# Performance work log

Hardware: AMD Instinct MI355X
Metric: run time of the kernel (lower is better)

The kernel has to match this reference:

```python
import jax, jax.numpy as jnp
import numpy as np

NEURONS = 4096
K = 512

def setup_inputs() -> dict:
    key = jax.random.key(0)
    s = jax.random.normal(key, (16384, NEURONS), dtype=jnp.float32)
    return {"s": s}

def reference(s) -> jnp.ndarray:
    # Original: sort each row ascending, zero the smallest (neurons - k) entries,
    # i.e. keep only the k largest values per row. With continuous random inputs
    # (no ties) this equals thresholding at the k-th largest value per row.
    topk_vals, _ = jax.lax.top_k(s, K)          # [B, K], descending
    thresh = topk_vals[:, -1:]                   # k-th largest per row, [B, 1]
    return jnp.where(s >= thresh, s, jnp.zeros((), dtype=s.dtype))
```

## Files before the change

### kernel.cpp

```cpp
#include <hip/hip_runtime.h>

#define ROWS 16384
#define COLS 4096
#define KSEL 512
#define THREADS 256
#define NCOPY0 8
#define HSTRIDE 260

__device__ __forceinline__ unsigned map_f(float f) {
    unsigned u = __float_as_uint(f);
    return u ^ (0x80000000u | (unsigned)((int)u >> 31));
}
__device__ __forceinline__ float unmap_f(unsigned m) {
    return __uint_as_float(m ^ (0x80000000u | ~(unsigned)((int)m >> 31)));
}

__device__ __forceinline__ void select_digit(unsigned n0, unsigned n1, unsigned n2,
                                             unsigned n3, int lane, int shift,
                                             unsigned& prefix, unsigned& kk) {
    unsigned ls3 = n3, ls2 = n3 + n2, ls1 = ls2 + n1, tot = ls1 + n0;
    unsigned S = tot;
#pragma unroll
    for (int off = 1; off < 64; off <<= 1) {
        unsigned o = __shfl(S, lane + off);
        S += (lane + off < 64) ? o : 0u;
    }
    const unsigned R = S - tot;
    const unsigned S3 = R + ls3, S2 = R + ls2, S1 = R + ls1, S0 = R + tot;
    unsigned dig = 0, nk = 0;
    bool found = false;
    if (S3 >= kk && R  < kk) { dig = 4 * lane + 3; nk = kk - R;  found = true; }
    if (S2 >= kk && S3 < kk) { dig = 4 * lane + 2; nk = kk - S3; found = true; }
    if (S1 >= kk && S2 < kk) { dig = 4 * lane + 1; nk = kk - S2; found = true; }
    if (S0 >= kk && S1 < kk) { dig = 4 * lane + 0; nk = kk - S1; found = true; }
    unsigned long long m = __ballot(found);
    int src = (int)__ffsll(m) - 1;
    prefix |= (unsigned)__shfl(dig, src) << shift;
    kk = (unsigned)__shfl(nk, src);
}

__global__ __launch_bounds__(THREADS, 8) void kwta_kernel(const float* __restrict__ in,
                                                          float* __restrict__ out) {
    __shared__ __align__(16) unsigned hist[(NCOPY0 + 3) * HSTRIDE];

    const int tid  = threadIdx.x;
    const int lane = tid & 63;
    const int row  = blockIdx.x;

    const float4* __restrict__ inrow  = (const float4*)(in  + (size_t)row * COLS);
    float4*       __restrict__ outrow = (float4*)(out + (size_t)row * COLS);

    unsigned v[16];
#pragma unroll
    for (int i = 0; i < 4; i++) {
        float4 f = inrow[tid + THREADS * i];
        v[4 * i + 0] = map_f(f.x);
        v[4 * i + 1] = map_f(f.y);
        v[4 * i + 2] = map_f(f.z);
        v[4 * i + 3] = map_f(f.w);
    }

    {
        const uint4 z = make_uint4(0u, 0u, 0u, 0u);
#pragma unroll
        for (int i = 0; i < 3; i++) {
            int w4 = tid + THREADS * i;
            if (w4 < (NCOPY0 + 3) * HSTRIDE / 4) ((uint4*)hist)[w4] = z;
        }
    }
    __syncthreads();

    unsigned prefix = 0;
    unsigned kk = KSEL;

    {
        unsigned* h0 = hist + (tid & (NCOPY0 - 1)) * HSTRIDE;
#pragma unroll
        for (int i = 0; i < 16; i++) atomicAdd(&h0[v[i] >> 24], 1u);
        __syncthreads();
        unsigned n0 = 0, n1 = 0, n2 = 0, n3 = 0;
#pragma unroll
        for (int c = 0; c < NCOPY0; c++) {
            uint4 t = ((const uint4*)(hist + c * HSTRIDE))[lane];
            n0 += t.x; n1 += t.y; n2 += t.z; n3 += t.w;
        }
        select_digit(n0, n1, n2, n3, lane, 24, prefix, kk);
    }

#pragma unroll
    for (int pass = 1; pass < 4; pass++) {
        const int shift = 24 - 8 * pass;
        const int hs = shift + 8;
        unsigned* hp = hist + (NCOPY0 + pass - 1) * HSTRIDE;
#pragma unroll
        for (int i = 0; i < 16; i++) {
            if (((v[i] ^ prefix) >> hs) == 0u)
                atomicAdd(&hp[(v[i] >> shift) & 255u], 1u);
        }
        __syncthreads();
        uint4 t = ((const uint4*)hp)[lane];
        select_digit(t.x, t.y, t.z, t.w, lane, shift, prefix, kk);
    }

#pragma unroll
    for (int i = 0; i < 4; i++) {
        float4 o;
        o.x = (v[4 * i + 0] >= prefix) ? unmap_f(v[4 * i + 0]) : 0.0f;
        o.y = (v[4 * i + 1] >= prefix) ? unmap_f(v[4 * i + 1]) : 0.0f;
        o.z = (v[4 * i + 2] >= prefix) ? unmap_f(v[4 * i + 2]) : 0.0f;
        o.w = (v[4 * i + 3] >= prefix) ? unmap_f(v[4 * i + 3]) : 0.0f;
        outrow[tid + THREADS * i] = o;
    }
}

extern "C" void kernel_launch(void* const* d_in, const int* in_sizes, int n_in,
                              void* d_out, int out_size, void* d_ws, size_t ws_size,
                              hipStream_t stream) {
    const float* s = (const float*)d_in[0];
    float* out = (float*)d_out;
    kwta_kernel<<<ROWS, THREADS, 0, stream>>>(s, out);
}
```

Baseline: 429.0 us.

## Use persistent blocks looping over rows with register prefetch of next row

The kernel now launches a fixed grid of 2048 blocks, and each block processes 8 rows strided by the grid size. While it runs the radix select on the current row, it prefetches the next row's data into registers. This is meant to hide global load latency behind the histogram and select work and to reduce block launch overhead. In exchange it uses more registers, which may lower occupancy, and adds an extra barrier per row for the histogram reset.

```diff
diff --git a/kernel.cpp b/kernel.cpp
--- a/kernel.cpp
+++ b/kernel.cpp
@@ -6,6 +6,8 @@
 #define THREADS 256
 #define NCOPY0 8
 #define HSTRIDE 260
+#define NBLOCKS 2048
+#define ROWS_PER_BLOCK (ROWS / NBLOCKS)
 
 __device__ __forceinline__ unsigned map_f(float f) {
     unsigned u = __float_as_uint(f);
@@ -45,71 +47,88 @@
 
     const int tid  = threadIdx.x;
     const int lane = tid & 63;
-    const int row  = blockIdx.x;
+    const int bid  = blockIdx.x;
 
-    const float4* __restrict__ inrow  = (const float4*)(in  + (size_t)row * COLS);
-    float4*       __restrict__ outrow = (float4*)(out + (size_t)row * COLS);
-
-    unsigned v[16];
+    float4 fnext[4];
+    {
+        const float4* __restrict__ p = (const float4*)(in + (size_t)bid * COLS);
 #pragma unroll
-    for (int i = 0; i < 4; i++) {
-        float4 f = inrow[tid + THREADS * i];
-        v[4 * i + 0] = map_f(f.x);
-        v[4 * i + 1] = map_f(f.y);
-        v[4 * i + 2] = map_f(f.z);
-        v[4 * i + 3] = map_f(f.w);
+        for (int i = 0; i < 4; i++) fnext[i] = p[tid + THREADS * i];
     }
 
-    {
-        const uint4 z = make_uint4(0u, 0u, 0u, 0u);
+#pragma unroll 1
+    for (int j = 0; j < ROWS_PER_BLOCK; j++) {
+        const size_t row = (size_t)j * NBLOCKS + bid;
+
+        unsigned v[16];
 #pragma unroll
-        for (int i = 0; i < 3; i++) {
-            int w4 = tid + THREADS * i;
-            if (w4 < (NCOPY0 + 3) * HSTRIDE / 4) ((uint4*)hist)[w4] = z;
+        for (int i = 0; i < 4; i++) {
+            v[4 * i + 0] = map_f(fnext[i].x);
+            v[4 * i + 1] = map_f(fnext[i].y);
+            v[4 * i + 2] = map_f(fnext[i].z);
+            v[4 * i + 3] = map_f(fnext[i].w);
         }
-    }
-    __syncthreads();
 
-    unsigned prefix = 0;
-    unsigned kk = KSEL;
+        if (j + 1 < ROWS_PER_BLOCK) {
+            const float4* __restrict__ p =
+                (const float4*)(in + ((size_t)(j + 1) * NBLOCKS + bid) * COLS);
+#pragma unroll
+            for (int i = 0; i < 4; i++) fnext[i] = p[tid + THREADS * i];
+        }
 
-    {
-        unsigned* h0 = hist + (tid & (NCOPY0 - 1)) * HSTRIDE;
+        __syncthreads();
+        {
+            const uint4 z = make_uint4(0u, 0u, 0u, 0u);
 #pragma unroll
-        for (int i = 0; i < 16; i++) atomicAdd(&h0[v[i] >> 24], 1u);
+            for (int i = 0; i < 3; i++) {
+                int w4 = tid + THREADS * i;
+                if (w4 < (NCOPY0 + 3) * HSTRIDE / 4) ((uint4*)hist)[w4] = z;
+            }
+        }
         __syncthreads();
-        unsigned n0 = 0, n1 = 0, n2 = 0, n3 = 0;
+
+        unsigned prefix = 0;
+        unsigned kk = KSEL;
+
+        {
+            unsigned* h0 = hist + (tid & (NCOPY0 - 1)) * HSTRIDE;
 #pragma unroll
-        for (int c = 0; c < NCOPY0; c++) {
-            uint4 t = ((const uint4*)(hist + c * HSTRIDE))[lane];
-            n0 += t.x; n1 += t.y; n2 += t.z; n3 += t.w;
+            for (int i = 0; i < 16; i++) atomicAdd(&h0[v[i] >> 24], 1u);
+            __syncthreads();
+            unsigned n0 = 0, n1 = 0, n2 = 0, n3 = 0;
+#pragma unroll
+            for (int c = 0; c < NCOPY0; c++) {
+                uint4 t = ((const uint4*)(hist + c * HSTRIDE))[lane];
+                n0 += t.x; n1 += t.y; n2 += t.z; n3 += t.w;
+            }
+            select_digit(n0, n1, n2, n3, lane, 24, prefix, kk);
         }
-        select_digit(n0, n1, n2, n3, lane, 24, prefix, kk);
-    }
 
 #pragma unroll
-    for (int pass = 1; pass < 4; pass++) {
-        const int shift = 24 - 8 * pass;
-        const int hs = shift + 8;
-        unsigned* hp = hist + (NCOPY0 + pass - 1) * HSTRIDE;
+        for (int pass = 1; pass < 4; pass++) {
+            const int shift = 24 - 8 * pass;
+            const int hs = shift + 8;
+            unsigned* hp = hist + (NCOPY0 + pass - 1) * HSTRIDE;
 #pragma unroll
-        for (int i = 0; i < 16; i++) {
-            if (((v[i] ^ prefix) >> hs) == 0u)
-                atomicAdd(&hp[(v[i] >> shift) & 255u], 1u);
+            for (int i = 0; i < 16; i++) {
+                if (((v[i] ^ prefix) >> hs) == 0u)
+                    atomicAdd(&hp[(v[i] >> shift) & 255u], 1u);
+            }
+            __syncthreads();
+            uint4 t = ((const uint4*)hp)[lane];
+            select_digit(t.x, t.y, t.z, t.w, lane, shift, prefix, kk);
         }
-        __syncthreads();
-        uint4 t = ((const uint4*)hp)[lane];
-        select_digit(t.x, t.y, t.z, t.w, lane, shift, prefix, kk);
-    }
 
+        float4* __restrict__ outrow = (float4*)(out + row * COLS);
 #pragma unroll
-    for (int i = 0; i < 4; i++) {
-        float4 o;
-        o.x = (v[4 * i + 0] >= prefix) ? unmap_f(v[4 * i + 0]) : 0.0f;
-        o.y = (v[4 * i + 1] >= prefix) ? unmap_f(v[4 * i + 1]) : 0.0f;
-        o.z = (v[4 * i + 2] >= prefix) ? unmap_f(v[4 * i + 2]) : 0.0f;
-        o.w = (v[4 * i + 3] >= prefix) ? unmap_f(v[4 * i + 3]) : 0.0f;
-        outrow[tid + THREADS * i] = o;
+        for (int i = 0; i < 4; i++) {
+            float4 o;
+            o.x = (v[4 * i + 0] >= prefix) ? unmap_f(v[4 * i + 0]) : 0.0f;
+            o.y = (v[4 * i + 1] >= prefix) ? unmap_f(v[4 * i + 1]) : 0.0f;
+            o.z = (v[4 * i + 2] >= prefix) ? unmap_f(v[4 * i + 2]) : 0.0f;
+            o.w = (v[4 * i + 3] >= prefix) ? unmap_f(v[4 * i + 3]) : 0.0f;
+            outrow[tid + THREADS * i] = o;
+        }
     }
 }
 
@@ -118,5 +137,5 @@
                               hipStream_t stream) {
     const float* s = (const float*)d_in[0];
     float* out = (float*)d_out;
-    kwta_kernel<<<ROWS, THREADS, 0, stream>>>(s, out);
+    kwta_kernel<<<NBLOCKS, THREADS, 0, stream>>>(s, out);
 }
```

Measured after the change: 507.7 us. +18.3%, slower.
